# Performance work log

Hardware: AMD Instinct MI355X
Metric: run time of the kernel (lower is better)

The kernel has to match this reference:

```python
import jax, jax.numpy as jnp
import numpy as np

N = 8192
TEMP = 0.5
EPS = 1e-12


def _normalize(z):
    # F.normalize(z, p=2, dim=1): x / max(||x||, eps)
    n = jnp.sqrt(jnp.sum(z * z, axis=1, keepdims=True))
    return z / jnp.maximum(n, EPS)


def _gcn(edge_index, edge_weight, x, w, b):
    # torch.sparse.mm(adj, x @ w): out[row] += adj[row, col] * support[col]
    support = x @ w
    msg = support[edge_index[1]] * edge_weight[:, None]
    return jax.ops.segment_sum(msg, edge_index[0], num_segments=N) + b


def _encoder(edge_index, edge_weight, feat, w_l1a, b_l1a, w_l1b, b_l1b, w_g1, b_g1, w_g2, b_g2):
    x = jax.nn.relu(feat @ w_l1a + b_l1a) @ w_l1b + b_l1b  # [N, 32]
    h = jax.nn.relu(_gcn(edge_index, edge_weight, x, w_g1, b_g1))  # [N, hid]
    return _gcn(edge_index, edge_weight, h, w_g2, b_g2)  # [N, act_fn]


def _proj(h, w_fc1, b_fc1, w_fc2, b_fc2):
    return jax.nn.elu(h @ w_fc1 + b_fc1) @ w_fc2 + b_fc2


def _loss(z1, z2):
    z1n = _normalize(z1)
    z2n = _normalize(z2)
    refl = jnp.exp((z1n @ z1n.T) / TEMP)      # [N, N]
    between = jnp.exp((z1n @ z2n.T) / TEMP)   # [N, N]
    denom = refl.sum(1) + between.sum(1) - jnp.diagonal(refl)
    return -jnp.log(jnp.diagonal(between) / denom)


def setup_inputs() -> dict:
    key = jax.random.key(0)
    ks = jax.random.split(key, 20)
    E = 262144
    in_dim, hid_dim, act_fn, out_dim = 512, 256, 128, 64

    def kaiming(k, shape):
        fan_in = shape[0]
        bound = np.sqrt(6.0 / fan_in)
        return jax.random.uniform(k, shape, jnp.float32, -bound, bound)

    return {
        "feat1": jax.random.normal(ks[0], (N, in_dim), jnp.float32),
        "feat2": jax.random.normal(ks[1], (N, in_dim), jnp.float32),
        "edge_index1": jax.random.randint(ks[2], (2, E), 0, N, jnp.int32),
        "edge_weight1": jax.random.uniform(ks[3], (E,), jnp.float32),
        "edge_index2": jax.random.randint(ks[4], (2, E), 0, N, jnp.int32),
        "edge_weight2": jax.random.uniform(ks[5], (E,), jnp.float32),
        "w_l1a": kaiming(ks[6], (in_dim, 64)),
        "b_l1a": jnp.zeros((64,), jnp.float32),
        "w_l1b": kaiming(ks[7], (64, 32)),
        "b_l1b": jnp.zeros((32,), jnp.float32),
        "w_g1": kaiming(ks[8], (32, hid_dim)),
        "b_g1": jnp.zeros((hid_dim,), jnp.float32),
        "w_g2": kaiming(ks[9], (hid_dim, act_fn)),
        "b_g2": jnp.zeros((act_fn,), jnp.float32),
        "w_fc1": kaiming(ks[10], (act_fn, out_dim)),
        "b_fc1": jnp.zeros((out_dim,), jnp.float32),
        "w_fc2": kaiming(ks[11], (out_dim, act_fn)),
        "b_fc2": jnp.zeros((act_fn,), jnp.float32),
    }


def reference(feat1, feat2, edge_index1, edge_weight1, edge_index2, edge_weight2,
              w_l1a, b_l1a, w_l1b, b_l1b, w_g1, b_g1, w_g2, b_g2,
              w_fc1, b_fc1, w_fc2, b_fc2):
    h1 = _encoder(edge_index1, edge_weight1, feat1, w_l1a, b_l1a, w_l1b, b_l1b, w_g1, b_g1, w_g2, b_g2)
    h2 = _encoder(edge_index2, edge_weight2, feat2, w_l1a, b_l1a, w_l1b, b_l1b, w_g1, b_g1, w_g2, b_g2)
    z1 = _proj(h1, w_fc1, b_fc1, w_fc2, b_fc2)
    z2 = _proj(h2, w_fc1, b_fc1, w_fc2, b_fc2)
    l1 = _loss(z1, z2)
    l2 = _loss(z2, z1)
    return ((l1 + l2) * 0.5).mean()
```

## Files before the change

kernel.cpp:

```cpp
#include <hip/hip_runtime.h>
#include <hip/hip_bf16.h>
#include <math.h>


#define NROWS 8192
#define MROWS 16384
#define NEDGE 262144

typedef __attribute__((ext_vector_type(8))) short bf16x8;
typedef __attribute__((ext_vector_type(4))) float f32x4;
typedef __attribute__((ext_vector_type(2))) float f32x2;
typedef __attribute__((ext_vector_type(8))) int i32x8;
typedef long long i64;

__device__ __forceinline__ short f2bf(float f){
  union { float f; unsigned u; } cv; cv.f = f;
  unsigned u = cv.u;
  unsigned r = (u + 0x7fffu + ((u >> 16) & 1u)) >> 16;
  return (short)r;
}
__device__ __forceinline__ f32x4 mfma16(bf16x8 a, bf16x8 b, f32x4 c){
  return __builtin_amdgcn_mfma_f32_16x16x32_bf16(a, b, c, 0, 0, 0);
}
__device__ __forceinline__ float fexp2(float x){
#if __has_builtin(__builtin_amdgcn_exp2f)
  return __builtin_amdgcn_exp2f(x);
#else
  return exp2f(x);
#endif
}

template<int CTRL>
__device__ __forceinline__ float dpp_add(float v){
  int s = __builtin_amdgcn_update_dpp(0, __builtin_bit_cast(int, v),
                                      CTRL, 0xf, 0xf, true);
  return v + __builtin_bit_cast(float, s);
}
__device__ __forceinline__ float red16(float v){
  v = dpp_add<0x101>(v);
  v = dpp_add<0x102>(v);
  v = dpp_add<0x104>(v);
  v = dpp_add<0x108>(v);
  return v;
}

__device__ unsigned char f2e4m3_sw(float f){
  float a = fabsf(f);
  unsigned s = (__float_as_uint(f)>>24)&0x80u;
  if (!(a>0.f)) return (unsigned char)s;
  if (a>448.f) a=448.f;
  int e; frexpf(a,&e);
  int eff=e-1;
  unsigned code;
  if (eff<-6){
    float q=rintf(a*512.f);
    code=(unsigned)q; if(code>7)code=7;
  } else {
    float q=rintf(a*exp2f((float)(3-eff)));
    unsigned mant=(unsigned)q;
    if(mant>=16){mant=8;eff++;}
    if(eff>8) return (unsigned char)(s|0x7e);
    code=((unsigned)(eff+7)<<3)|(mant-8);
  }
  return (unsigned char)(s|code);
}
__device__ __forceinline__ unsigned short pack2fp8(float a, float b){
#if __has_builtin(__builtin_amdgcn_cvt_pk_fp8_f32)
  int v = __builtin_amdgcn_cvt_pk_fp8_f32(a, b, 0, false);
  return (unsigned short)(v & 0xffff);
#else
  return (unsigned short)((unsigned)f2e4m3_sw(a) | ((unsigned)f2e4m3_sw(b)<<8));
#endif
}

struct WtArgs {
  const float* src[6];
  short* dst[6];
  int K[6], N[6];
  int off[7];
  int nwt;
};
__global__ void setup_k(WtArgs a, const int* __restrict__ ei1, const int* __restrict__ ei2,
                        int* __restrict__ deg1, int* __restrict__ deg2){
  int b = blockIdx.x;
  if (b < a.nwt){
    int i = b*256 + threadIdx.x;
    if (i >= a.off[6]) return;
    int s = 0;
    #pragma unroll
    for (int j=1;j<6;j++) if (i >= a.off[j]) s=j;
    int l = i - a.off[s];
    int K=a.K[s], N=a.N[s];
    int k=l/N, n=l-k*N;
    a.dst[s][(long)n*K+k] = f2bf(a.src[s][l]);
  } else {
    int hb = b - a.nwt;
    const int* ei = (hb < NEDGE/256) ? ei1 : ei2;
    int* deg = (hb < NEDGE/256) ? deg1 : deg2;
    int e = (hb % (NEDGE/256))*256 + threadIdx.x;
    atomicAdd(&deg[ei[e]], 1);
  }
}

__global__ void scan2_k(const int* __restrict__ deg1, int* __restrict__ rs1, int* __restrict__ cur1,
                        const int* __restrict__ deg2, int* __restrict__ rs2, int* __restrict__ cur2){
  const int* deg = blockIdx.x ? deg2 : deg1;
  int* rowstart = blockIdx.x ? rs2 : rs1;
  int* cursor = blockIdx.x ? cur2 : cur1;
  __shared__ int csum[256];
  int t = threadIdx.x;
  int loc[32];
  int s = 0;
  for (int j=0;j<32;j++){ int d = deg[t*32+j]; loc[j] = s; s += d; }
  int v = s;
  csum[t] = v;
  __syncthreads();
  for (int st=1; st<256; st<<=1){
    int o = (t >= st) ? csum[t-st] : 0;
    __syncthreads();
    v += o;
    csum[t] = v;
    __syncthreads();
  }
  int base = v - s;
  for (int j=0;j<32;j++){ int w = base + loc[j]; rowstart[t*32+j]=w; cursor[t*32+j]=w; }
  if (t==255) rowstart[NROWS] = v;
}

__global__ __launch_bounds__(256) void fm_k(const float* __restrict__ F0, const float* __restrict__ F1,
    const short* __restrict__ Wa, const float* __restrict__ ba,
    const short* __restrict__ Wb, const float* __restrict__ bb, short* __restrict__ xb,
    const int* __restrict__ ei1, const float* __restrict__ w1, int* __restrict__ cur1,
    int* __restrict__ ecol1, float* __restrict__ ew1,
    const int* __restrict__ ei2, const float* __restrict__ w2, int* __restrict__ cur2,
    int* __restrict__ ecol2, float* __restrict__ ew2){
  __shared__ short As[32*520];
  __shared__ short a1s[32*72];
  const int tid = threadIdx.x;
  if (blockIdx.x >= MROWS/32){
    int b = blockIdx.x - MROWS/32;
    bool g2 = (b >= NEDGE/256);
    const int* ei = g2 ? ei2 : ei1;
    const float* w = g2 ? w2 : w1;
    int* cursor = g2 ? cur2 : cur1;
    int* ecol = g2 ? ecol2 : ecol1;
    float* ew = g2 ? ew2 : ew1;
    int e = (b % (NEDGE/256))*256 + tid;
    int r = ei[e];
    int p = atomicAdd(&cursor[r], 1);
    ecol[p] = ei[NEDGE + e];
    ew[p] = w[e];
    return;
  }
  const int m0 = blockIdx.x*32;
  const float* F = (m0 < NROWS) ? (F0 + (long)m0*512) : (F1 + (long)(m0-NROWS)*512);
  {
    float4 st[16];
    #pragma unroll
    for (int i=0;i<16;i++) st[i] = *(const float4*)(F + (long)(i*256+tid)*4);
    #pragma unroll
    for (int i=0;i<16;i++){
      int idx = i*256+tid, row = idx>>7, c4 = idx&127;
      unsigned lo = (unsigned)(unsigned short)f2bf(st[i].x) | ((unsigned)(unsigned short)f2bf(st[i].y)<<16);
      unsigned hi = (unsigned)(unsigned short)f2bf(st[i].z) | ((unsigned)(unsigned short)f2bf(st[i].w)<<16);
      uint2 o = {lo, hi};
      *(uint2*)&As[row*520 + c4*4] = o;
    }
  }
  __syncthreads();
  const int wave = tid>>6, lane = tid&63, quad = lane>>4, cl = lane&15;
  f32x4 zero = {0.f,0.f,0.f,0.f};
  {
    const int wno = wave*16;
    f32x4 acc[2] = {zero, zero};
    #pragma unroll
    for (int kc=0;kc<16;kc++){
      const int ko = kc*32 + quad*8;
      bf16x8 a0 = *(const bf16x8*)&As[(cl)*520 + ko];
      bf16x8 a1 = *(const bf16x8*)&As[(16+cl)*520 + ko];
      bf16x8 b = *(const bf16x8*)(Wa + (long)(wno + cl)*512 + ko);
      acc[0] = mfma16(a0, b, acc[0]);
      acc[1] = mfma16(a1, b, acc[1]);
    }
    int col = wno + cl;
    float bv = ba[col];
    #pragma unroll
    for (int mt=0;mt<2;mt++)
      #pragma unroll
      for (int r=0;r<4;r++)
        a1s[(mt*16 + quad*4 + r)*72 + col] = f2bf(fmaxf(acc[mt][r] + bv, 0.f));
  }
  __syncthreads();
  if (wave < 2){
    f32x4 acc2[2] = {zero, zero};
    #pragma unroll
    for (int kc=0;kc<2;kc++){
      const int ko = kc*32 + quad*8;
      bf16x8 a = *(const bf16x8*)&a1s[(wave*16+cl)*72 + ko];
      #pragma unroll
      for (int nt=0;nt<2;nt++){
        bf16x8 b = *(const bf16x8*)(Wb + (long)(nt*16 + cl)*64 + ko);
        acc2[nt] = mfma16(a, b, acc2[nt]);
      }
    }
    #pragma unroll
    for (int nt=0;nt<2;nt++){
      int col = nt*16 + cl;
      float bv = bb[col];
      #pragma unroll
      for (int r=0;r<4;r++)
        xb[(long)(m0 + wave*16 + quad*4 + r)*32 + col] = f2bf(acc2[nt][r] + bv);
    }
  }
}

__device__ __forceinline__ void acc8(float* acc, int4 v, float f){
  const unsigned* u = (const unsigned*)&v;
  #pragma unroll
  for (int i=0;i<4;i++){
    union{unsigned x; float y;} lo, hi;
    lo.x = u[i] << 16;
    hi.x = u[i] & 0xffff0000u;
    acc[2*i]   = fmaf(f, lo.y, acc[2*i]);
    acc[2*i+1] = fmaf(f, hi.y, acc[2*i+1]);
  }
}
template<int C>
__device__ __forceinline__ void gather_row(float* acc, const short* sb,
                                           const int* ec, const float* w, int s, int e){
  int k = s;
  for (; k+16 <= e; k+=16){
    int c[16]; float f[16]; int4 v[16];
    #pragma unroll
    for (int u=0;u<16;u++){ c[u]=ec[k+u]; f[u]=w[k+u]; }
    #pragma unroll
    for (int u=0;u<16;u++) v[u] = *(const int4*)(sb + (long)c[u]*C);
    #pragma unroll
    for (int u=0;u<16;u++) acc8(acc, v[u], f[u]);
  }
  for (; k+4 <= e; k+=4){
    int c0=ec[k],c1=ec[k+1],c2=ec[k+2],c3=ec[k+3];
    float f0=w[k],f1=w[k+1],f2=w[k+2],f3=w[k+3];
    int4 v0 = *(const int4*)(sb + (long)c0*C);
    int4 v1 = *(const int4*)(sb + (long)c1*C);
    int4 v2 = *(const int4*)(sb + (long)c2*C);
    int4 v3 = *(const int4*)(sb + (long)c3*C);
    acc8(acc,v0,f0); acc8(acc,v1,f1); acc8(acc,v2,f2); acc8(acc,v3,f3);
  }
  for (; k < e; k++){
    int4 v0 = *(const int4*)(sb + (long)ec[k]*C);
    acc8(acc,v0,w[k]);
  }
}

__global__ __launch_bounds__(256) void gg_k(const short* __restrict__ xb,
    const int* __restrict__ rs1, const int* __restrict__ ec1, const float* __restrict__ w1,
    const int* __restrict__ rs2, const int* __restrict__ ec2, const float* __restrict__ w2,
    const short* __restrict__ Wg1, const float* __restrict__ bg1,
    const short* __restrict__ Wg2, short* __restrict__ s2){
  __shared__ short axs[64*40];
  __shared__ short hbs[64*264];
  const int tid = threadIdx.x;
  const int m0 = blockIdx.x*64;
  {
    const int g = tid & 3, sub = tid >> 2;
    const int row = m0 + sub;
    const int* rs; const int* ec; const float* w; int soff, lr;
    if (row < NROWS){ rs=rs1; ec=ec1; w=w1; soff=0; lr=row; }
    else            { rs=rs2; ec=ec2; w=w2; soff=NROWS; lr=row-NROWS; }
    const short* sb = xb + (long)soff*32 + g*8;
    float acc[8];
    #pragma unroll
    for (int j=0;j<8;j++) acc[j] = 0.f;
    gather_row<32>(acc, sb, ec, w, rs[lr], rs[lr+1]);
    int4 ov;
    unsigned* ou = (unsigned*)&ov;
    #pragma unroll
    for (int i=0;i<4;i++)
      ou[i] = (unsigned)(unsigned short)f2bf(acc[2*i]) | ((unsigned)(unsigned short)f2bf(acc[2*i+1])<<16);
    *(int4*)&axs[sub*40 + g*8] = ov;
  }
  __syncthreads();
  const int wave = tid>>6, lane = tid&63, quad = lane>>4, cl = lane&15;
  f32x4 zero = {0.f,0.f,0.f,0.f};
  {
    const int wno = wave*64;
    f32x4 acc[4][4];
    #pragma unroll
    for (int i=0;i<4;i++)
      #pragma unroll
      for (int j=0;j<4;j++) acc[i][j]=zero;
    const int ko = quad*8;
    bf16x8 a[4], b[4];
    #pragma unroll
    for (int mt=0;mt<4;mt++)
      a[mt] = *(const bf16x8*)&axs[(mt*16+cl)*40 + ko];
    #pragma unroll
    for (int nt=0;nt<4;nt++)
      b[nt] = *(const bf16x8*)(Wg1 + (long)(wno + nt*16 + cl)*32 + ko);
    #pragma unroll
    for (int mt=0;mt<4;mt++)
      #pragma unroll
      for (int nt=0;nt<4;nt++)
        acc[mt][nt] = mfma16(a[mt], b[nt], acc[mt][nt]);
    #pragma unroll
    for (int nt=0;nt<4;nt++){
      int col = wno + nt*16 + cl;
      float bv = bg1[col];
      #pragma unroll
      for (int mt=0;mt<4;mt++)
        #pragma unroll
        for (int r=0;r<4;r++)
          hbs[(mt*16 + quad*4 + r)*264 + col] = f2bf(fmaxf(acc[mt][nt][r] + bv, 0.f));
    }
  }
  __syncthreads();
  {
    const int wno = wave*32;
    f32x4 acc[4][2];
    #pragma unroll
    for (int i=0;i<4;i++){ acc[i][0]=zero; acc[i][1]=zero; }
    #pragma unroll
    for (int kc=0;kc<8;kc++){
      const int ko = kc*32 + quad*8;
      bf16x8 a[4], b[2];
      #pragma unroll
      for (int mt=0;mt<4;mt++)
        a[mt] = *(const bf16x8*)&hbs[(mt*16+cl)*264 + ko];
      #pragma unroll
      for (int nt=0;nt<2;nt++)
        b[nt] = *(const bf16x8*)(Wg2 + (long)(wno + nt*16 + cl)*256 + ko);
      #pragma unroll
      for (int mt=0;mt<4;mt++)
        #pragma unroll
        for (int nt=0;nt<2;nt++)
          acc[mt][nt] = mfma16(a[mt], b[nt], acc[mt][nt]);
    }
    #pragma unroll
    for (int mt=0;mt<4;mt++)
      #pragma unroll
      for (int nt=0;nt<2;nt++){
        int col = wno + nt*16 + cl;
        #pragma unroll
        for (int r=0;r<4;r++)
          s2[(long)(m0 + mt*16 + quad*4 + r)*128 + col] = f2bf(acc[mt][nt][r]);
      }
  }
}

__global__ __launch_bounds__(256) void pn_k(const short* __restrict__ s2,
    const int* __restrict__ rs1, const int* __restrict__ ec1, const float* __restrict__ w1,
    const int* __restrict__ rs2, const int* __restrict__ ec2, const float* __restrict__ w2,
    const float* __restrict__ bg2,
    const short* __restrict__ Wf1, const float* __restrict__ bf1,
    const short* __restrict__ Wf2, const float* __restrict__ bf2,
    unsigned short* __restrict__ Zf, float* __restrict__ bdot){
  __shared__ short hs[64*136];
  __shared__ short t2s[64*72];
  __shared__ float zs[64*132];
  __shared__ float sp[4][64];
  __shared__ float dp[4][32];
  __shared__ float rnS[64];
  const float SQKE = 1.6986436f;
  const int tid = threadIdx.x;
  const int wave = tid>>6, lane = tid&63, quad = lane>>4, cl = lane&15;
  const int m0h = blockIdx.x*32;
  {
    const int g = tid & 15, sub = tid >> 4;
    #pragma unroll 1
    for (int pass=0; pass<4; pass++){
      int hrow = pass*16 + sub;
      int lr = m0h + (hrow & 31);
      const int* rs; const int* ec; const float* w; long soff;
      if (hrow < 32){ rs=rs1; ec=ec1; w=w1; soff=0; }
      else          { rs=rs2; ec=ec2; w=w2; soff=NROWS; }
      const short* sb = s2 + soff*128 + g*8;
      float acc[8];
      #pragma unroll
      for (int j=0;j<8;j++) acc[j] = bg2[g*8+j];
      gather_row<128>(acc, sb, ec, w, rs[lr], rs[lr+1]);
      int4 ov;
      unsigned* ou = (unsigned*)&ov;
      #pragma unroll
      for (int i=0;i<4;i++)
        ou[i] = (unsigned)(unsigned short)f2bf(acc[2*i]) | ((unsigned)(unsigned short)f2bf(acc[2*i+1])<<16);
      *(int4*)&hs[hrow*136 + g*8] = ov;
    }
  }
  __syncthreads();
  f32x4 zero = {0.f,0.f,0.f,0.f};
  {
    const int wno = wave*16;
    f32x4 acc[4];
    #pragma unroll
    for (int i=0;i<4;i++) acc[i]=zero;
    #pragma unroll
    for (int kc=0;kc<4;kc++){
      const int ko = kc*32 + quad*8;
      bf16x8 a[4], b;
      #pragma unroll
      for (int mt=0;mt<4;mt++)
        a[mt] = *(const bf16x8*)&hs[(mt*16+cl)*136 + ko];
      b = *(const bf16x8*)(Wf1 + (long)(wno + cl)*128 + ko);
      #pragma unroll
      for (int mt=0;mt<4;mt++) acc[mt] = mfma16(a[mt], b, acc[mt]);
    }
    int col = wno + cl;
    float bv = bf1[col];
    #pragma unroll
    for (int mt=0;mt<4;mt++)
      #pragma unroll
      for (int r=0;r<4;r++){
        float v = acc[mt][r] + bv;
        v = (v > 0.f) ? v : expm1f(v);
        t2s[(mt*16 + quad*4 + r)*72 + col] = f2bf(v);
      }
  }
  __syncthreads();
  {
    const int wno = wave*32;
    f32x4 acc[4][2];
    #pragma unroll
    for (int i=0;i<4;i++){ acc[i][0]=zero; acc[i][1]=zero; }
    #pragma unroll
    for (int kc=0;kc<2;kc++){
      const int ko = kc*32 + quad*8;
      bf16x8 a[4], b[2];
      #pragma unroll
      for (int mt=0;mt<4;mt++)
        a[mt] = *(const bf16x8*)&t2s[(mt*16+cl)*72 + ko];
      #pragma unroll
      for (int nt=0;nt<2;nt++)
        b[nt] = *(const bf16x8*)(Wf2 + (long)(wno + nt*16 + cl)*64 + ko);
      #pragma unroll
      for (int mt=0;mt<4;mt++)
        #pragma unroll
        for (int nt=0;nt<2;nt++)
          acc[mt][nt] = mfma16(a[mt], b[nt], acc[mt][nt]);
    }
    #pragma unroll
    for (int mt=0;mt<4;mt++)
      #pragma unroll
      for (int nt=0;nt<2;nt++){
        int col = wno + nt*16 + cl;
        float bv = bf2[col];
        #pragma unroll
        for (int r=0;r<4;r++)
          zs[(mt*16 + quad*4 + r)*132 + col] = acc[mt][nt][r] + bv;
      }
  }
  __syncthreads();
  {
    int row = tid & 63, qtr = tid >> 6;
    const float* zr = &zs[row*132 + qtr*32];
    float s = 0.f;
    #pragma unroll 8
    for (int c=0;c<32;c++) s += zr[c]*zr[c];
    sp[qtr][row] = s;
    if (row < 32){
      const float* zb_ = &zs[(row+32)*132 + qtr*32];
      float d = 0.f;
      #pragma unroll 8
      for (int c=0;c<32;c++) d += zr[c]*zb_[c];
      dp[qtr][row] = d;
    }
  }
  __syncthreads();
  if (tid < 64){
    float ssq = sp[0][tid]+sp[1][tid]+sp[2][tid]+sp[3][tid];
    rnS[tid] = 1.f / fmaxf(sqrtf(ssq), 1e-12f);
  }
  __syncthreads();
  if (tid < 32){
    float dot = dp[0][tid]+dp[1][tid]+dp[2][tid]+dp[3][tid];
    bdot[m0h + tid] = dot * rnS[tid] * rnS[tid+32];
  }
  {
    int lr = tid >> 2;
    int grow = (lr < 32) ? (m0h + lr) : (NROWS + m0h + lr - 32);
    float s = rnS[lr] * SQKE;
    int p0 = (tid & 3)*16;
    long gbase = (long)(grow>>4)*1024 + (long)(grow&15)*16 + (long)(p0>>4)*256;
    #pragma unroll
    for (int pp=0;pp<16;pp++){
      int p = p0 + pp;
      Zf[gbase + pp] = pack2fp8(zs[lr*132 + 2*p]*s, zs[lr*132 + 2*p + 1]*s);
    }
  }
}

__global__ __launch_bounds__(256,4) void gram3_k(const unsigned char* __restrict__ Zf,
                                                 float* __restrict__ P){
  __shared__ float srow[4][64];
  __shared__ float scol[4][64];
  const int wave = threadIdx.x>>6, lane = threadIdx.x&63;
  const int t = blockIdx.x*4 + wave;
  int ti = (int)((513.0f - sqrtf(513.0f*513.0f - 8.0f*(float)t))*0.5f);
  while ((ti+1)*256 - ((ti+1)*ti)/2 <= t) ti++;
  while (ti*256 - (ti*(ti-1))/2 > t) ti--;
  const int tj = ti + (t - (ti*256 - (ti*(ti-1))/2));
  const unsigned char* za = Zf + (long)ti*8192 + lane*32;
  const unsigned char* zb = Zf + (long)tj*8192 + lane*32;
  const int quad = lane>>4, cl = lane&15;

  f32x4 zero = {0.f,0.f,0.f,0.f};
  f32x2 z2 = {0.f,0.f};
  f32x2 cs[4] = {z2,z2,z2,z2};

  i32x8 Bf[4];
  #pragma unroll
  for (int nt=0;nt<4;nt++)
    Bf[nt] = *(const i32x8*)(zb + nt*2048);

  i32x8 Ab[2];
  Ab[0] = *(const i32x8*)(za);
  Ab[1] = *(const i32x8*)(za + 2048);

  auto exprow = [&](const f32x4* ar, int mt){
    f32x2 r01 = z2, r23 = z2;
    #pragma unroll
    for (int nt=0;nt<4;nt++){
      f32x4 v = ar[nt];
      float e0 = fexp2(v[0]), e1 = fexp2(v[1]);
      float e2 = fexp2(v[2]), e3 = fexp2(v[3]);
      f32x2 p01 = {e0,e1}, p23 = {e2,e3};
      r01 += p01; r23 += p23;
      cs[nt] += p01; cs[nt] += p23;
    }
    float s0 = red16(r01.x);
    float s1 = red16(r01.y);
    float s2 = red16(r23.x);
    float s3 = red16(r23.y);
    if (cl==0){
      f32x4 rv = {s0, s1, s2, s3};
      *(f32x4*)&srow[wave][mt*16 + quad*4] = rv;
    }
  };

  const int SC1 = 0x7F;
  f32x4 acc2[2][4];
  #pragma unroll
  for (int nt=0;nt<4;nt++)
    acc2[0][nt] = __builtin_amdgcn_mfma_scale_f32_16x16x128_f8f6f4(
        Ab[0], Bf[nt], zero, 0, 0, 0, SC1, 0, SC1);
  #pragma unroll
  for (int mt=1; mt<4; mt++){
    const int cur = mt&1, prv = cur^1;
    if (mt<3)
      Ab[prv] = *(const i32x8*)(za + (mt+1)*2048);
    #pragma unroll
    for (int nt=0;nt<4;nt++)
      acc2[cur][nt] = __builtin_amdgcn_mfma_scale_f32_16x16x128_f8f6f4(
          Ab[cur], Bf[nt], zero, 0, 0, 0, SC1, 0, SC1);
    exprow(&acc2[prv][0], mt-1);
  }
  exprow(&acc2[1][0], 3);

  __threadfence_block();
  P[((long)ti*256 + tj)*64 + lane] = srow[wave][lane];
  if (ti != tj){
    #pragma unroll
    for (int nt=0;nt<4;nt++){
      float s = cs[nt].x + cs[nt].y;
      s += __shfl_xor(s,16); s += __shfl_xor(s,32);
      if (quad==0) scol[wave][nt*16 + cl] = s;
    }
    __threadfence_block();
    P[((long)tj*256 + ti)*64 + lane] = scol[wave][lane];
  }
}

__global__ __launch_bounds__(256) void rloss_k(const float* __restrict__ P,
                                               const float* __restrict__ bdot,
                                               float* __restrict__ out){
  __shared__ float ps[8][32][2];
  const float E2 = 7.3890560989306495f;
  int t = threadIdx.x;
  int rloc = t & 31, grp = t >> 5;
  int i = blockIdx.x*32 + rloc;
  int j = i + NROWS;
  const float* p1 = P + (long)(i>>6)*256*64 + (long)grp*32*64 + (i&63);
  const float* p2 = P + (long)(j>>6)*256*64 + (long)grp*32*64 + (j&63);
  float s1 = 0.f, s2 = 0.f;
  #pragma unroll 8
  for (int b=0;b<32;b++){ s1 += p1[b*64]; s2 += p2[b*64]; }
  ps[grp][rloc][0] = s1;
  ps[grp][rloc][1] = s2;
  __syncthreads();
  if (t < 64){
    float term = 0.f;
    if (t < 32){
      float a1 = 0.f, a2 = 0.f;
      #pragma unroll
      for (int g=0; g<8; g++){ a1 += ps[g][t][0]; a2 += ps[g][t][1]; }
      int ii = blockIdx.x*32 + t;
      float lb = 2.f * bdot[ii];
      term = 0.5f * ((logf(a1 - E2) - lb) + (logf(a2 - E2) - lb));
    }
    #pragma unroll
    for (int m=1; m<64; m<<=1) term += __shfl_xor(term, m);
    if (t==0) atomicAdd(out, term / (float)NROWS);
  }
}

extern "C" void kernel_launch(void* const* d_in, const int* in_sizes, int n_in,
                              void* d_out, int out_size, void* d_ws, size_t ws_size,
                              hipStream_t stream){
  const float* feat1 = (const float*)d_in[0];
  const float* feat2 = (const float*)d_in[1];
  const int*   ei1   = (const int*)d_in[2];
  const float* w1    = (const float*)d_in[3];
  const int*   ei2   = (const int*)d_in[4];
  const float* w2    = (const float*)d_in[5];
  const float* w_l1a = (const float*)d_in[6];
  const float* b_l1a = (const float*)d_in[7];
  const float* w_l1b = (const float*)d_in[8];
  const float* b_l1b = (const float*)d_in[9];
  const float* w_g1  = (const float*)d_in[10];
  const float* b_g1  = (const float*)d_in[11];
  const float* w_g2  = (const float*)d_in[12];
  const float* b_g2  = (const float*)d_in[13];
  const float* w_fc1 = (const float*)d_in[14];
  const float* b_fc1 = (const float*)d_in[15];
  const float* w_fc2 = (const float*)d_in[16];
  const float* b_fc2 = (const float*)d_in[17];

  float* P = (float*)d_ws;
  char* base = (char*)d_ws;
  size_t off = (size_t)17<<20;
  auto alloc = [&](size_t bytes)->void*{
    void* r = base + off;
    off = (off + bytes + 255) & ~(size_t)255;
    return r;
  };
  short* xb   = (short*)alloc((size_t)MROWS*32*2);
  short* s2   = (short*)alloc((size_t)MROWS*128*2);
  short* wl1a_t = (short*)alloc(512*64*2);
  short* wl1b_t = (short*)alloc(64*32*2);
  short* wg1_t  = (short*)alloc(32*256*2);
  short* wg2_t  = (short*)alloc(256*128*2);
  short* wfc1_t = (short*)alloc(128*64*2);
  short* wfc2_t = (short*)alloc(64*128*2);
  unsigned short* Zf = (unsigned short*)alloc((size_t)MROWS*128);
  int*   deg1 = (int*)alloc(NROWS*4);
  int*   deg2 = (int*)alloc(NROWS*4);
  int* rs1  = (int*)alloc((NROWS+1)*4);
  int* cur1 = (int*)alloc(NROWS*4);
  int* rs2  = (int*)alloc((NROWS+1)*4);
  int* cur2 = (int*)alloc(NROWS*4);
  int*   ecol1 = (int*)alloc((size_t)NEDGE*4);
  float* ewt1  = (float*)alloc((size_t)NEDGE*4);
  int*   ecol2 = (int*)alloc((size_t)NEDGE*4);
  float* ewt2  = (float*)alloc((size_t)NEDGE*4);
  float* bdot  = (float*)alloc(NROWS*4);

  hipMemsetAsync(deg1, 0, (size_t)2*NROWS*4, stream);
  hipMemsetAsync(d_out, 0, sizeof(float), stream);

  WtArgs wa;
  wa.src[0]=w_l1a; wa.dst[0]=wl1a_t; wa.K[0]=512; wa.N[0]=64;
  wa.src[1]=w_l1b; wa.dst[1]=wl1b_t; wa.K[1]=64;  wa.N[1]=32;
  wa.src[2]=w_g1;  wa.dst[2]=wg1_t;  wa.K[2]=32;  wa.N[2]=256;
  wa.src[3]=w_g2;  wa.dst[3]=wg2_t;  wa.K[3]=256; wa.N[3]=128;
  wa.src[4]=w_fc1; wa.dst[4]=wfc1_t; wa.K[4]=128; wa.N[4]=64;
  wa.src[5]=w_fc2; wa.dst[5]=wfc2_t; wa.K[5]=64;  wa.N[5]=128;
  wa.off[0]=0;
  for (int i=0;i<6;i++) wa.off[i+1] = wa.off[i] + wa.K[i]*wa.N[i];
  wa.nwt = (wa.off[6]+255)/256;

  setup_k<<<wa.nwt + 2*(NEDGE/256),256,0,stream>>>(wa, ei1, ei2, deg1, deg2);
  scan2_k<<<2,256,0,stream>>>(deg1, rs1, cur1, deg2, rs2, cur2);
  fm_k<<<MROWS/32 + 2*(NEDGE/256),256,0,stream>>>(feat1, feat2, wl1a_t, b_l1a,
      wl1b_t, b_l1b, xb,
      ei1, w1, cur1, ecol1, ewt1,
      ei2, w2, cur2, ecol2, ewt2);
  gg_k<<<MROWS/64,256,0,stream>>>(xb, rs1,ecol1,ewt1, rs2,ecol2,ewt2,
                                  wg1_t, b_g1, wg2_t, s2);
  pn_k<<<NROWS/32,256,0,stream>>>(s2, rs1,ecol1,ewt1, rs2,ecol2,ewt2, b_g2,
                                  wfc1_t, b_fc1, wfc2_t, b_fc2, Zf, bdot);
  gram3_k<<<8224,256,0,stream>>>((const unsigned char*)Zf, P);
  rloss_k<<<NROWS/32,256,0,stream>>>(P, bdot, (float*)d_out);
}
```

Baseline: 247.6 us.

## Interleave CSR column and weight into int2, batch edge scatter per thread

Stores each CSR edge's column index and weight together as one int2 record instead of two separate arrays. The gathers in gg_k and pn_k then read one 8-byte load per edge, not two 4-byte loads. The edge-fill blocks now handle 8 edges per thread with batched atomics, and they are placed first in the fm_k grid so they start before the feature-matmul blocks. This cuts fill block count and gather load instructions, at the cost of larger per-thread register use in the fill path.

```diff
diff --git a/kernel.cpp b/kernel.cpp
--- a/kernel.cpp
+++ b/kernel.cpp
@@ -6,6 +6,8 @@
 #define NROWS 8192
 #define MROWS 16384
 #define NEDGE 262144
+#define EPT 8
+#define NFILLB (2*(NEDGE/(256*EPT)))
 
 typedef __attribute__((ext_vector_type(8))) short bf16x8;
 typedef __attribute__((ext_vector_type(4))) float f32x4;
@@ -131,28 +133,36 @@
     const short* __restrict__ Wa, const float* __restrict__ ba,
     const short* __restrict__ Wb, const float* __restrict__ bb, short* __restrict__ xb,
     const int* __restrict__ ei1, const float* __restrict__ w1, int* __restrict__ cur1,
-    int* __restrict__ ecol1, float* __restrict__ ew1,
+    int2* __restrict__ eg1,
     const int* __restrict__ ei2, const float* __restrict__ w2, int* __restrict__ cur2,
-    int* __restrict__ ecol2, float* __restrict__ ew2){
+    int2* __restrict__ eg2){
   __shared__ short As[32*520];
   __shared__ short a1s[32*72];
   const int tid = threadIdx.x;
-  if (blockIdx.x >= MROWS/32){
-    int b = blockIdx.x - MROWS/32;
-    bool g2 = (b >= NEDGE/256);
+  if (blockIdx.x < NFILLB){
+    int b = blockIdx.x;
+    bool g2 = (b >= NFILLB/2);
     const int* ei = g2 ? ei2 : ei1;
     const float* w = g2 ? w2 : w1;
     int* cursor = g2 ? cur2 : cur1;
-    int* ecol = g2 ? ecol2 : ecol1;
-    float* ew = g2 ? ew2 : ew1;
-    int e = (b % (NEDGE/256))*256 + tid;
-    int r = ei[e];
-    int p = atomicAdd(&cursor[r], 1);
-    ecol[p] = ei[NEDGE + e];
-    ew[p] = w[e];
+    int2* eg = g2 ? eg2 : eg1;
+    int e0 = (b % (NFILLB/2))*(256*EPT) + tid;
+    int r[EPT]; int c[EPT]; float wv[EPT];
+    #pragma unroll
+    for (int u=0;u<EPT;u++){
+      int e = e0 + u*256;
+      r[u] = ei[e];
+      c[u] = ei[NEDGE + e];
+      wv[u] = w[e];
+    }
+    int p[EPT];
+    #pragma unroll
+    for (int u=0;u<EPT;u++) p[u] = atomicAdd(&cursor[r[u]], 1);
+    #pragma unroll
+    for (int u=0;u<EPT;u++) eg[p[u]] = make_int2(c[u], __float_as_int(wv[u]));
     return;
   }
-  const int m0 = blockIdx.x*32;
+  const int m0 = (blockIdx.x - NFILLB)*32;
   const float* F = (m0 < NROWS) ? (F0 + (long)m0*512) : (F1 + (long)(m0-NROWS)*512);
   {
     float4 st[16];
@@ -227,35 +237,36 @@
 }
 template<int C>
 __device__ __forceinline__ void gather_row(float* acc, const short* sb,
-                                           const int* ec, const float* w, int s, int e){
+                                           const int2* eg, int s, int e){
   int k = s;
   for (; k+16 <= e; k+=16){
-    int c[16]; float f[16]; int4 v[16];
-    #pragma unroll
-    for (int u=0;u<16;u++){ c[u]=ec[k+u]; f[u]=w[k+u]; }
-    #pragma unroll
-    for (int u=0;u<16;u++) v[u] = *(const int4*)(sb + (long)c[u]*C);
-    #pragma unroll
-    for (int u=0;u<16;u++) acc8(acc, v[u], f[u]);
+    int2 cw[16]; int4 v[16];
+    #pragma unroll
+    for (int u=0;u<16;u++) cw[u] = eg[k+u];
+    #pragma unroll
+    for (int u=0;u<16;u++) v[u] = *(const int4*)(sb + (long)cw[u].x*C);
+    #pragma unroll
+    for (int u=0;u<16;u++) acc8(acc, v[u], __int_as_float(cw[u].y));
   }
   for (; k+4 <= e; k+=4){
-    int c0=ec[k],c1=ec[k+1],c2=ec[k+2],c3=ec[k+3];
-    float f0=w[k],f1=w[k+1],f2=w[k+2],f3=w[k+3];
-    int4 v0 = *(const int4*)(sb + (long)c0*C);
-    int4 v1 = *(const int4*)(sb + (long)c1*C);
-    int4 v2 = *(const int4*)(sb + (long)c2*C);
-    int4 v3 = *(const int4*)(sb + (long)c3*C);
-    acc8(acc,v0,f0); acc8(acc,v1,f1); acc8(acc,v2,f2); acc8(acc,v3,f3);
+    int2 c0=eg[k], c1=eg[k+1], c2=eg[k+2], c3=eg[k+3];
+    int4 v0 = *(const int4*)(sb + (long)c0.x*C);
+    int4 v1 = *(const int4*)(sb + (long)c1.x*C);
+    int4 v2 = *(const int4*)(sb + (long)c2.x*C);
+    int4 v3 = *(const int4*)(sb + (long)c3.x*C);
+    acc8(acc,v0,__int_as_float(c0.y)); acc8(acc,v1,__int_as_float(c1.y));
+    acc8(acc,v2,__int_as_float(c2.y)); acc8(acc,v3,__int_as_float(c3.y));
   }
   for (; k < e; k++){
-    int4 v0 = *(const int4*)(sb + (long)ec[k]*C);
-    acc8(acc,v0,w[k]);
+    int2 c0 = eg[k];
+    int4 v0 = *(const int4*)(sb + (long)c0.x*C);
+    acc8(acc,v0,__int_as_float(c0.y));
   }
 }
 
 __global__ __launch_bounds__(256) void gg_k(const short* __restrict__ xb,
-    const int* __restrict__ rs1, const int* __restrict__ ec1, const float* __restrict__ w1,
-    const int* __restrict__ rs2, const int* __restrict__ ec2, const float* __restrict__ w2,
+    const int* __restrict__ rs1, const int2* __restrict__ eg1,
+    const int* __restrict__ rs2, const int2* __restrict__ eg2,
     const short* __restrict__ Wg1, const float* __restrict__ bg1,
     const short* __restrict__ Wg2, short* __restrict__ s2){
   __shared__ short axs[64*40];
@@ -265,14 +276,14 @@
   {
     const int g = tid & 3, sub = tid >> 2;
     const int row = m0 + sub;
-    const int* rs; const int* ec; const float* w; int soff, lr;
-    if (row < NROWS){ rs=rs1; ec=ec1; w=w1; soff=0; lr=row; }
-    else            { rs=rs2; ec=ec2; w=w2; soff=NROWS; lr=row-NROWS; }
+    const int* rs; const int2* eg; int soff, lr;
+    if (row < NROWS){ rs=rs1; eg=eg1; soff=0; lr=row; }
+    else            { rs=rs2; eg=eg2; soff=NROWS; lr=row-NROWS; }
     const short* sb = xb + (long)soff*32 + g*8;
     float acc[8];
     #pragma unroll
     for (int j=0;j<8;j++) acc[j] = 0.f;
-    gather_row<32>(acc, sb, ec, w, rs[lr], rs[lr+1]);
+    gather_row<32>(acc, sb, eg, rs[lr], rs[lr+1]);
     int4 ov;
     unsigned* ou = (unsigned*)&ov;
     #pragma unroll
@@ -349,8 +360,8 @@
 }
 
 __global__ __launch_bounds__(256) void pn_k(const short* __restrict__ s2,
-    const int* __restrict__ rs1, const int* __restrict__ ec1, const float* __restrict__ w1,
-    const int* __restrict__ rs2, const int* __restrict__ ec2, const float* __restrict__ w2,
+    const int* __restrict__ rs1, const int2* __restrict__ eg1,
+    const int* __restrict__ rs2, const int2* __restrict__ eg2,
     const float* __restrict__ bg2,
     const short* __restrict__ Wf1, const float* __restrict__ bf1,
     const short* __restrict__ Wf2, const float* __restrict__ bf2,
@@ -371,14 +382,14 @@
     for (int pass=0; pass<4; pass++){
       int hrow = pass*16 + sub;
       int lr = m0h + (hrow & 31);
-      const int* rs; const int* ec; const float* w; long soff;
-      if (hrow < 32){ rs=rs1; ec=ec1; w=w1; soff=0; }
-      else          { rs=rs2; ec=ec2; w=w2; soff=NROWS; }
+      const int* rs; const int2* eg; long soff;
+      if (hrow < 32){ rs=rs1; eg=eg1; soff=0; }
+      else          { rs=rs2; eg=eg2; soff=NROWS; }
       const short* sb = s2 + soff*128 + g*8;
       float acc[8];
       #pragma unroll
       for (int j=0;j<8;j++) acc[j] = bg2[g*8+j];
-      gather_row<128>(acc, sb, ec, w, rs[lr], rs[lr+1]);
+      gather_row<128>(acc, sb, eg, rs[lr], rs[lr+1]);
       int4 ov;
       unsigned* ou = (unsigned*)&ov;
       #pragma unroll
@@ -648,10 +659,8 @@
   int* cur1 = (int*)alloc(NROWS*4);
   int* rs2  = (int*)alloc((NROWS+1)*4);
   int* cur2 = (int*)alloc(NROWS*4);
-  int*   ecol1 = (int*)alloc((size_t)NEDGE*4);
-  float* ewt1  = (float*)alloc((size_t)NEDGE*4);
-  int*   ecol2 = (int*)alloc((size_t)NEDGE*4);
-  float* ewt2  = (float*)alloc((size_t)NEDGE*4);
+  int2*  eg1 = (int2*)alloc((size_t)NEDGE*8);
+  int2*  eg2 = (int2*)alloc((size_t)NEDGE*8);
   float* bdot  = (float*)alloc(NROWS*4);
 
   hipMemsetAsync(deg1, 0, (size_t)2*NROWS*4, stream);
@@ -670,13 +679,13 @@
 
   setup_k<<<wa.nwt + 2*(NEDGE/256),256,0,stream>>>(wa, ei1, ei2, deg1, deg2);
   scan2_k<<<2,256,0,stream>>>(deg1, rs1, cur1, deg2, rs2, cur2);
-  fm_k<<<MROWS/32 + 2*(NEDGE/256),256,0,stream>>>(feat1, feat2, wl1a_t, b_l1a,
+  fm_k<<<NFILLB + MROWS/32,256,0,stream>>>(feat1, feat2, wl1a_t, b_l1a,
       wl1b_t, b_l1b, xb,
-      ei1, w1, cur1, ecol1, ewt1,
-      ei2, w2, cur2, ecol2, ewt2);
-  gg_k<<<MROWS/64,256,0,stream>>>(xb, rs1,ecol1,ewt1, rs2,ecol2,ewt2,
+      ei1, w1, cur1, eg1,
+      ei2, w2, cur2, eg2);
+  gg_k<<<MROWS/64,256,0,stream>>>(xb, rs1,eg1, rs2,eg2,
                                   wg1_t, b_g1, wg2_t, s2);
-  pn_k<<<NROWS/32,256,0,stream>>>(s2, rs1,ecol1,ewt1, rs2,ecol2,ewt2, b_g2,
+  pn_k<<<NROWS/32,256,0,stream>>>(s2, rs1,eg1, rs2,eg2, b_g2,
                                   wfc1_t, b_fc1, wfc2_t, b_fc2, Zf, bdot);
   gram3_k<<<8224,256,0,stream>>>((const unsigned char*)Zf, P);
   rloss_k<<<NROWS/32,256,0,stream>>>(P, bdot, (float*)d_out);
```

Measured after the change: 253.4 us. 1.02x slower.
